# Performance work log

Measured on AMD Instinct MI355X. Metric: run time of the kernel, lower is better.

The kernel has to match this reference:

```python
import jax, jax.numpy as jnp
import numpy as np

NUM_HEADS = 16
KEY_SIZE = 64
VALUE_SIZE = 64
D_MODEL = 1024
B, S = 2, 2048

def setup_inputs() -> dict:
    key = jax.random.key(0)
    k1, k2 = jax.random.split(key)
    inputs = jax.random.normal(k1, (B, S, D_MODEL), dtype=jnp.float32)
    qkv_width = NUM_HEADS * (KEY_SIZE + KEY_SIZE + VALUE_SIZE)  # 3072
    W = jax.random.normal(k2, (D_MODEL, qkv_width), dtype=jnp.float32) / np.sqrt(D_MODEL)
    b = jnp.zeros((qkv_width,), dtype=jnp.float32)
    return {"inputs": inputs, "W": W, "b": b}

def reference(inputs, W, b):
    # Fused QKV projection: [B, S, H*(2k+v)]
    qkv = jnp.einsum("bsd,de->bse", inputs, W) + b
    Bsz, S_ = inputs.shape[0], inputs.shape[1]
    qkv = qkv.reshape(Bsz, S_, NUM_HEADS, 2 * KEY_SIZE + VALUE_SIZE)
    qkv = jnp.transpose(qkv, (0, 2, 1, 3))  # [B, H, S, 2k+v]
    q = qkv[..., :KEY_SIZE]
    k = qkv[..., KEY_SIZE:2 * KEY_SIZE]
    v = qkv[..., 2 * KEY_SIZE:]
    # NOTE: original multiplies by sqrt(key_size) (not divide) -- faithful.
    scores = jnp.einsum("bhqd,bhkd->bhqk", q, k) * jnp.sqrt(jnp.float32(KEY_SIZE))
    weights = jax.nn.softmax(scores, axis=-1)
    out = jnp.einsum("bhqk,bhkv->bhqv", weights, v)  # [B, H, S, v]
    out = jnp.transpose(out, (0, 2, 1, 3)).reshape(Bsz, S_, NUM_HEADS * VALUE_SIZE)
    return out
```

## Files before the change

kernel.cpp:

```cpp
#include <hip/hip_runtime.h>


#define S_LEN 2048
#define NH    16
#define DH    64
#define DM    1024
#define EW    3072
#define NROWS 4096
#define NT    32

#define QSCALE 11.5415603f

using f32x4 = __attribute__((ext_vector_type(4))) float;
using bf8   = __attribute__((ext_vector_type(8))) short;
using s4v   = __attribute__((ext_vector_type(4))) short;

static __device__ __forceinline__ short f2bf(float f) {
  union { float f; unsigned u; } a; a.f = f;
  unsigned r = a.u + 0x7fffu + ((a.u >> 16) & 1u);
  return (short)(r >> 16);
}
static __device__ __forceinline__ float bf2f(short h) {
  union { float f; unsigned u; } a;
  a.u = ((unsigned)(unsigned short)h) << 16;
  return a.f;
}
static __device__ __forceinline__ unsigned fbits(float f) {
  union { float f; unsigned u; } a; a.f = f; return a.u;
}
static __device__ __forceinline__ void gl16(const void* g, void* l) {
  __builtin_amdgcn_global_load_lds(
      (const __attribute__((address_space(1))) void*)g,
      (__attribute__((address_space(3))) void*)l, 16, 0, 0);
}

__global__ __launch_bounds__(256) void prep_x(const float* __restrict__ X,
                                              short* __restrict__ Xh,
                                              short* __restrict__ Xl) {
  int i = blockIdx.x * 256 + threadIdx.x;
  float4 v = ((const float4*)X)[i];
  s4v h, l;
  h.x = f2bf(v.x); l.x = f2bf(v.x - bf2f(h.x));
  h.y = f2bf(v.y); l.y = f2bf(v.y - bf2f(h.y));
  h.z = f2bf(v.z); l.z = f2bf(v.z - bf2f(h.z));
  h.w = f2bf(v.w); l.w = f2bf(v.w - bf2f(h.w));
  ((s4v*)Xh)[i] = h;
  ((s4v*)Xl)[i] = l;
}

__global__ __launch_bounds__(256) void prep_w(const float* __restrict__ W,
                                              short* __restrict__ Wth,
                                              short* __restrict__ Wtl) {
  __shared__ float t[32][33];
  int n0 = blockIdx.x * 32;
  int k0 = blockIdx.y * 32;
  int tx = threadIdx.x & 31;
  int ty = threadIdx.x >> 5;
#pragma unroll
  for (int i = 0; i < 32; i += 8)
    t[ty + i][tx] = W[(size_t)(k0 + ty + i) * EW + n0 + tx];
  __syncthreads();
#pragma unroll
  for (int i = 0; i < 32; i += 8) {
    float v = t[tx][ty + i];
    int n = n0 + ty + i;
    int h = n / 192, e = n - h * 192;
    int np = (e < 64) ? (h * 64 + e)
           : (e < 128) ? (1024 + h * 64 + (e - 64))
                       : (2048 + h * 64 + (e - 128));
    short hi = f2bf(v);
    short lo = f2bf(v - bf2f(hi));
    size_t o = (size_t)np * DM + k0 + tx;
    Wth[o] = hi; Wtl[o] = lo;
  }
}

__global__ __launch_bounds__(256, 2) void proj_qk(
    const short* __restrict__ Xh, const short* __restrict__ Xl,
    const short* __restrict__ Wth, const short* __restrict__ Wtl,
    const float* __restrict__ bias,
    short* __restrict__ Qh, short* __restrict__ Ql,
    short* __restrict__ Kh, short* __restrict__ Kl) {
  __shared__ short Ah[2][4096], Al[2][4096], Bh[2][4096], Bl[2][4096];
  const int tid = threadIdx.x;
  const int lane = tid & 63, w = tid >> 6;
  const int wr = w >> 1, wc = w & 1;
  const int c = lane & 15, g = lane >> 4;

  const int id = blockIdx.x;
  const int t = id >> 3;
  const int rowBase = (((id & 7) << 2) + (t & 3)) * 128;
  const int colBase = (t >> 2) * 128;

  f32x4 acc[4][4] = {};

  const int sr  = 32 * w + (lane >> 2);
  const int csw = ((lane & 3) ^ ((lane >> 3) & 3)) * 8;
  const int ldsw = w * 1024;
  const size_t aBase = (size_t)(rowBase + sr) * DM + csw;
  const size_t bBase = (size_t)(colBase + sr) * DM + csw;

  const int rsw = (g ^ ((c >> 1) & 3)) * 8;

#define PSTAGE(B, kt) do {                                    \
    gl16(&Xh[aBase + (kt)],            &Ah[B][ldsw]);         \
    gl16(&Xh[aBase + (kt) + 16 * DM],  &Ah[B][ldsw + 512]);   \
    gl16(&Xl[aBase + (kt)],            &Al[B][ldsw]);         \
    gl16(&Xl[aBase + (kt) + 16 * DM],  &Al[B][ldsw + 512]);   \
    gl16(&Wth[bBase + (kt)],           &Bh[B][ldsw]);         \
    gl16(&Wth[bBase + (kt) + 16 * DM], &Bh[B][ldsw + 512]);   \
    gl16(&Wtl[bBase + (kt)],           &Bl[B][ldsw]);         \
    gl16(&Wtl[bBase + (kt) + 16 * DM], &Bl[B][ldsw + 512]);   \
  } while (0)

  PSTAGE(0, 0);
  __syncthreads();

  for (int it = 0; it < 32; ++it) {
    const int cur = it & 1;

    bf8 ah[4], al4[4], bh[4], bl[4];
#pragma unroll
    for (int m = 0; m < 4; ++m) {
      int ro = (wr * 64 + m * 16 + c) * 32 + rsw;
      ah[m]  = *(const bf8*)&Ah[cur][ro];
      al4[m] = *(const bf8*)&Al[cur][ro];
    }
#pragma unroll
    for (int n = 0; n < 4; ++n) {
      int ro = (wc * 64 + n * 16 + c) * 32 + rsw;
      bh[n] = *(const bf8*)&Bh[cur][ro];
      bl[n] = *(const bf8*)&Bl[cur][ro];
    }
    if (it + 1 < 32) PSTAGE(cur ^ 1, (it + 1) * 32);

    __builtin_amdgcn_s_setprio(1);
#pragma unroll
    for (int m = 0; m < 4; ++m)
#pragma unroll
      for (int n = 0; n < 4; ++n) {
        acc[m][n] = __builtin_amdgcn_mfma_f32_16x16x32_bf16(al4[m], bh[n], acc[m][n], 0, 0, 0);
        acc[m][n] = __builtin_amdgcn_mfma_f32_16x16x32_bf16(ah[m], bl[n], acc[m][n], 0, 0, 0);
        acc[m][n] = __builtin_amdgcn_mfma_f32_16x16x32_bf16(ah[m], bh[n], acc[m][n], 0, 0, 0);
      }
    __builtin_amdgcn_s_setprio(0);
    __syncthreads();
  }
#undef PSTAGE

#pragma unroll
  for (int m = 0; m < 4; ++m)
#pragma unroll
    for (int n = 0; n < 4; ++n)
#pragma unroll
      for (int j = 0; j < 4; ++j) {
        int grow = rowBase + wr * 64 + m * 16 + g * 4 + j;
        int gcol = colBase + wc * 64 + n * 16 + c;
        int h = (gcol >> 6) & 15, e = gcol & 63;
        int bb = grow >> 11, s = grow & 2047;
        size_t hb = (size_t)(bb * NH + h);
        if (gcol < 1024) {
          float q8 = (acc[m][n][j] + bias[h * 192 + e]) * QSCALE;
          short hi = f2bf(q8);
          short lo = f2bf(q8 - bf2f(hi));
          size_t idx = (hb * S_LEN + s) * DH + e;
          Qh[idx] = hi; Ql[idx] = lo;
        } else {
          float v = acc[m][n][j] + bias[h * 192 + 64 + e];
          short hi = f2bf(v);
          short lo = f2bf(v - bf2f(hi));
          int tile = s >> 6, r = s & 63;
          size_t idx = ((hb * NT + tile) * (size_t)4096) + r * 64 +
                       ((((e >> 3) ^ (r & 7)) << 3) | (e & 7));
          Kh[idx] = hi; Kl[idx] = lo;
        }
      }
}

__global__ __launch_bounds__(256, 2) void proj_v(
    const short* __restrict__ Xh, const short* __restrict__ Wth,
    const float* __restrict__ bias, short* __restrict__ Vt) {
  __shared__ short Ah[2][4096], Bh[2][4096];
  const int tid = threadIdx.x;
  const int lane = tid & 63, w = tid >> 6;
  const int wr = w >> 1, wc = w & 1;
  const int c = lane & 15, g = lane >> 4;

  const int id = blockIdx.x;
  const int t = id >> 3;
  const int rowBase = (((id & 7) << 2) + (t & 3)) * 128;
  const int colBase = 2048 + (t >> 2) * 128;

  f32x4 acc[4][4] = {};

  const int sr  = 32 * w + (lane >> 2);
  const int csw = ((lane & 3) ^ ((lane >> 3) & 3)) * 8;
  const int ldsw = w * 1024;
  const size_t aBase = (size_t)(rowBase + sr) * DM + csw;
  const size_t bBase = (size_t)(colBase + sr) * DM + csw;
  const int rsw = (g ^ ((c >> 1) & 3)) * 8;

#define VSTAGE(B, kt) do {                                    \
    gl16(&Xh[aBase + (kt)],            &Ah[B][ldsw]);         \
    gl16(&Xh[aBase + (kt) + 16 * DM],  &Ah[B][ldsw + 512]);   \
    gl16(&Wth[bBase + (kt)],           &Bh[B][ldsw]);         \
    gl16(&Wth[bBase + (kt) + 16 * DM], &Bh[B][ldsw + 512]);   \
  } while (0)

  VSTAGE(0, 0);
  __syncthreads();

  for (int it = 0; it < 32; ++it) {
    const int cur = it & 1;
    bf8 ah[4], bh[4];
#pragma unroll
    for (int m = 0; m < 4; ++m)
      ah[m] = *(const bf8*)&Ah[cur][(wr * 64 + m * 16 + c) * 32 + rsw];
#pragma unroll
    for (int n = 0; n < 4; ++n)
      bh[n] = *(const bf8*)&Bh[cur][(wc * 64 + n * 16 + c) * 32 + rsw];
    if (it + 1 < 32) VSTAGE(cur ^ 1, (it + 1) * 32);

    __builtin_amdgcn_s_setprio(1);
#pragma unroll
    for (int m = 0; m < 4; ++m)
#pragma unroll
      for (int n = 0; n < 4; ++n)
        acc[m][n] = __builtin_amdgcn_mfma_f32_16x16x32_bf16(ah[m], bh[n], acc[m][n], 0, 0, 0);
    __builtin_amdgcn_s_setprio(0);
    __syncthreads();
  }
#undef VSTAGE

#pragma unroll
  for (int m = 0; m < 4; ++m)
#pragma unroll
    for (int n = 0; n < 4; ++n)
#pragma unroll
      for (int j = 0; j < 4; ++j) {
        int grow = rowBase + wr * 64 + m * 16 + g * 4 + j;
        int gcol = colBase + wc * 64 + n * 16 + c;
        int h = (gcol >> 6) & 15, d = gcol & 63;
        int bb = grow >> 11, s = grow & 2047;
        size_t hb = (size_t)(bb * NH + h);
        float v = acc[m][n][j] + bias[h * 192 + 128 + d];
        int tile = s >> 6, key = s & 63;
        int kc = key >> 5, g4 = (key >> 2) & 3;
        int ii = (((key >> 4) & 1) << 2) | (key & 3);
        size_t idx = ((hb * NT + tile) * (size_t)4096) + d * 64 +
                     (((((kc << 2) | g4) ^ (d & 7)) << 3) | ii);
        Vt[idx] = f2bf(v);
      }
}

__global__ __launch_bounds__(512, 4) void attn(
    const short* __restrict__ Qh, const short* __restrict__ Ql,
    const short* __restrict__ KhG, const short* __restrict__ KlG,
    const short* __restrict__ VtG, float* __restrict__ out) {
  __shared__ short KHs[2][4096];
  __shared__ short KLs[2][4096];
  __shared__ short Vs[2][4096];

  const int tid = threadIdx.x;
  const int lane = tid & 63, w = tid >> 6;
  const int c = lane & 15, g = lane >> 4;
  const int id = blockIdx.x;
  const int lid = (id & 7) * 64 + (id >> 3);
  const int bh = lid >> 4;
  const int q0 = (lid & 15) * 128 + w * 16;
  const size_t qBase  = (size_t)bh * S_LEN * DH;
  const size_t kvBase = (size_t)bh * NT * 4096;

  const int seg = tid * 8;

  bf8 qh[2], ql[2];
#pragma unroll
  for (int kc = 0; kc < 2; ++kc) {
    size_t idx = qBase + (size_t)(q0 + c) * DH + kc * 32 + g * 8;
    qh[kc] = *(const bf8*)&Qh[idx];
    ql[kc] = *(const bf8*)&Ql[idx];
  }

  int koff[2][4];
#pragma unroll
  for (int kc = 0; kc < 2; ++kc)
#pragma unroll
    for (int i = 0; i < 4; ++i)
      koff[kc][i] = (i * 16 + c) * 64 + (((kc * 4 + g) ^ (c & 7)) << 3);

  float mrun = -INFINITY, lpart = 0.f;
  f32x4 o[4] = {};

  gl16(&KhG[kvBase + seg], &KHs[0][seg]);
  gl16(&KlG[kvBase + seg], &KLs[0][seg]);
  gl16(&VtG[kvBase + seg], &Vs[0][seg]);
  __syncthreads();

  for (int t = 0; t < NT; ++t) {
    const int cur = t & 1, nxt = cur ^ 1;
    if (t + 1 < NT) {
      size_t tb = kvBase + (size_t)(t + 1) * 4096 + seg;
      gl16(&KhG[tb], &KHs[nxt][seg]);
      gl16(&KlG[tb], &KLs[nxt][seg]);
      gl16(&VtG[tb], &Vs[nxt][seg]);
    }
    const short* KH = &KHs[cur][0];
    const short* KL = &KLs[cur][0];
    const short* VV = &Vs[cur][0];

    f32x4 sc[4];
    __builtin_amdgcn_s_setprio(1);
#pragma unroll
    for (int nb = 0; nb < 4; ++nb) {
      f32x4 s = {};
#pragma unroll
      for (int kc = 0; kc < 2; ++kc) {
        bf8 kh = *(const bf8*)&KH[koff[kc][nb]];
        bf8 kl = *(const bf8*)&KL[koff[kc][nb]];
        s = __builtin_amdgcn_mfma_f32_16x16x32_bf16(kh, ql[kc], s, 0, 0, 0);
        s = __builtin_amdgcn_mfma_f32_16x16x32_bf16(kl, qh[kc], s, 0, 0, 0);
        s = __builtin_amdgcn_mfma_f32_16x16x32_bf16(kh, qh[kc], s, 0, 0, 0);
      }
      sc[nb] = s;
    }
    __builtin_amdgcn_s_setprio(0);

    float m0 = fmaxf(fmaxf(sc[0][0], sc[0][1]), fmaxf(sc[0][2], sc[0][3]));
#pragma unroll
    for (int nb = 1; nb < 4; ++nb)
      m0 = fmaxf(m0, fmaxf(fmaxf(sc[nb][0], sc[nb][1]),
                           fmaxf(sc[nb][2], sc[nb][3])));
    m0 = fmaxf(m0, __shfl_xor(m0, 16));
    m0 = fmaxf(m0, __shfl_xor(m0, 32));

    if (__any(m0 > mrun + 8.0f)) {
      float mnew = fmaxf(mrun, m0);
      float scale = exp2f(mrun - mnew);
      mrun = mnew;
      lpart *= scale;
      int sb = (g << 4) | (g << 2);
      float s0 = __shfl(scale, sb);
      float s1 = __shfl(scale, sb + 1);
      float s2 = __shfl(scale, sb + 2);
      float s3 = __shfl(scale, sb + 3);
#pragma unroll
      for (int db = 0; db < 4; ++db) {
        o[db][0] *= s0; o[db][1] *= s1; o[db][2] *= s2; o[db][3] *= s3;
      }
    }

#pragma unroll
    for (int nb = 0; nb < 4; ++nb)
#pragma unroll
      for (int j = 0; j < 4; ++j)
        sc[nb][j] = exp2f(sc[nb][j] - mrun);
#pragma unroll
    for (int nb = 0; nb < 4; ++nb)
      lpart += (sc[nb][0] + sc[nb][1]) + (sc[nb][2] + sc[nb][3]);

    union { bf8 v; unsigned u[4]; } pa[2];
#pragma unroll
    for (int kc = 0; kc < 2; ++kc) {
      pa[kc].u[0] = (fbits(sc[2*kc][0]) >> 16)   | (fbits(sc[2*kc][1])   & 0xffff0000u);
      pa[kc].u[1] = (fbits(sc[2*kc][2]) >> 16)   | (fbits(sc[2*kc][3])   & 0xffff0000u);
      pa[kc].u[2] = (fbits(sc[2*kc+1][0]) >> 16) | (fbits(sc[2*kc+1][1]) & 0xffff0000u);
      pa[kc].u[3] = (fbits(sc[2*kc+1][2]) >> 16) | (fbits(sc[2*kc+1][3]) & 0xffff0000u);
    }

    __builtin_amdgcn_s_setprio(1);
#pragma unroll
    for (int kc = 0; kc < 2; ++kc)
#pragma unroll
      for (int db = 0; db < 4; ++db) {
        bf8 vb = *(const bf8*)&VV[koff[kc][db]];
        o[db] = __builtin_amdgcn_mfma_f32_16x16x32_bf16(pa[kc].v, vb, o[db], 0, 0, 0);
      }
    __builtin_amdgcn_s_setprio(0);

    __syncthreads();
  }

  lpart += __shfl_xor(lpart, 16);
  lpart += __shfl_xor(lpart, 32);
  int sb = (g << 4) | (g << 2);
  float r0 = 1.f / __shfl(lpart, sb);
  float r1 = 1.f / __shfl(lpart, sb + 1);
  float r2 = 1.f / __shfl(lpart, sb + 2);
  float r3 = 1.f / __shfl(lpart, sb + 3);

  const int b = bh >> 4, h = bh & 15;
#pragma unroll
  for (int db = 0; db < 4; ++db) {
    int col = h * DH + db * 16 + c;
    out[((size_t)b * S_LEN + q0 + g * 4 + 0) * DM + col] = o[db][0] * r0;
    out[((size_t)b * S_LEN + q0 + g * 4 + 1) * DM + col] = o[db][1] * r1;
    out[((size_t)b * S_LEN + q0 + g * 4 + 2) * DM + col] = o[db][2] * r2;
    out[((size_t)b * S_LEN + q0 + g * 4 + 3) * DM + col] = o[db][3] * r3;
  }
}

extern "C" void kernel_launch(void* const* d_in, const int* in_sizes, int n_in,
                              void* d_out, int out_size, void* d_ws, size_t ws_size,
                              hipStream_t stream) {
  const float* X    = (const float*)d_in[0];
  const float* W    = (const float*)d_in[1];
  const float* bias = (const float*)d_in[2];
  float* out = (float*)d_out;

  char* ws = (char*)d_ws;
  size_t off = 0;
  auto take = [&](size_t bytes) {
    void* p = ws + off;
    off += (bytes + 255) & ~(size_t)255;
    return p;
  };
  short* Xh  = (short*)take((size_t)NROWS * DM * 2);
  short* Xl  = (short*)take((size_t)NROWS * DM * 2);
  short* Wth = (short*)take((size_t)EW * DM * 2);
  short* Wtl = (short*)take((size_t)EW * DM * 2);
  short* Qh  = (short*)take((size_t)2 * NH * S_LEN * DH * 2);
  short* Ql  = (short*)take((size_t)2 * NH * S_LEN * DH * 2);
  short* Kh  = (short*)take((size_t)2 * NH * NT * 4096 * 2);
  short* Kl  = (short*)take((size_t)2 * NH * NT * 4096 * 2);
  short* Vt  = (short*)take((size_t)2 * NH * NT * 4096 * 2);

  prep_x<<<dim3(4096), dim3(256), 0, stream>>>(X, Xh, Xl);
  prep_w<<<dim3(EW / 32, DM / 32), dim3(256), 0, stream>>>(W, Wth, Wtl);
  proj_qk<<<dim3(512), dim3(256), 0, stream>>>(
      Xh, Xl, Wth, Wtl, bias, Qh, Ql, Kh, Kl);
  proj_v<<<dim3(256), dim3(256), 0, stream>>>(Xh, Wth, bias, Vt);
  attn<<<dim3(512), dim3(512), 0, stream>>>(
      Qh, Ql, Kh, Kl, Vt, out);
}
```

Before: 174.5 us.

## Pre-swizzle W into MFMA fragment layout and load B operands directly to registers

prep_w now writes the bf16 weight halves in a fragment-major layout matching the MFMA B operand. The projection kernels read B straight from global memory into registers, one k-step ahead, instead of staging it through LDS, which halves LDS traffic and footprint. The low half of W is no longer written for V columns, and the main loop is unrolled by two. Separately, the attention P-matrix packing switches from truncating bit masks to the v_cvt_pk_bf16_f32 instruction, which rounds to nearest, slightly changing numerics. Each lane's 16-byte global loads are contiguous in the new layout, but register pressure rises from holding two sets of B fragments.

After: 174.6 us. About the same (+0.0%).

```diff
diff --git a/kernel.cpp b/kernel.cpp
--- a/kernel.cpp
+++ b/kernel.cpp
@@ -24,9 +24,6 @@
   union { float f; unsigned u; } a;
   a.u = ((unsigned)(unsigned short)h) << 16;
   return a.f;
-}
-static __device__ __forceinline__ unsigned fbits(float f) {
-  union { float f; unsigned u; } a; a.f = f; return a.u;
 }
 static __device__ __forceinline__ void gl16(const void* g, void* l) {
   __builtin_amdgcn_global_load_lds(
@@ -49,8 +46,8 @@
 }
 
 __global__ __launch_bounds__(256) void prep_w(const float* __restrict__ W,
-                                              short* __restrict__ Wth,
-                                              short* __restrict__ Wtl) {
+                                              short* __restrict__ Wfh,
+                                              short* __restrict__ Wfl) {
   __shared__ float t[32][33];
   int n0 = blockIdx.x * 32;
   int k0 = blockIdx.y * 32;
@@ -60,6 +57,7 @@
   for (int i = 0; i < 32; i += 8)
     t[ty + i][tx] = W[(size_t)(k0 + ty + i) * EW + n0 + tx];
   __syncthreads();
+  const int kt = k0 >> 5;
 #pragma unroll
   for (int i = 0; i < 32; i += 8) {
     float v = t[tx][ty + i];
@@ -68,20 +66,22 @@
     int np = (e < 64) ? (h * 64 + e)
            : (e < 128) ? (1024 + h * 64 + (e - 64))
                        : (2048 + h * 64 + (e - 128));
+    int n16 = np >> 4, c = np & 15;
+    int gg = (tx >> 3) & 3, ee = tx & 7;
+    size_t o = ((size_t)(n16 * 32 + kt)) * 512 + (gg * 16 + c) * 8 + ee;
     short hi = f2bf(v);
-    short lo = f2bf(v - bf2f(hi));
-    size_t o = (size_t)np * DM + k0 + tx;
-    Wth[o] = hi; Wtl[o] = lo;
+    Wfh[o] = hi;
+    if (np < 2048) Wfl[o] = f2bf(v - bf2f(hi));
   }
 }
 
 __global__ __launch_bounds__(256, 2) void proj_qk(
     const short* __restrict__ Xh, const short* __restrict__ Xl,
-    const short* __restrict__ Wth, const short* __restrict__ Wtl,
+    const short* __restrict__ Wfh, const short* __restrict__ Wfl,
     const float* __restrict__ bias,
     short* __restrict__ Qh, short* __restrict__ Ql,
     short* __restrict__ Kh, short* __restrict__ Kl) {
-  __shared__ short Ah[2][4096], Al[2][4096], Bh[2][4096], Bl[2][4096];
+  __shared__ short Ah[2][4096], Al[2][4096];
   const int tid = threadIdx.x;
   const int lane = tid & 63, w = tid >> 6;
   const int wr = w >> 1, wc = w & 1;
@@ -98,55 +98,74 @@
   const int csw = ((lane & 3) ^ ((lane >> 3) & 3)) * 8;
   const int ldsw = w * 1024;
   const size_t aBase = (size_t)(rowBase + sr) * DM + csw;
-  const size_t bBase = (size_t)(colBase + sr) * DM + csw;
-
   const int rsw = (g ^ ((c >> 1) & 3)) * 8;
 
-#define PSTAGE(B, kt) do {                                    \
+  size_t bB[4];
+#pragma unroll
+  for (int n = 0; n < 4; ++n)
+    bB[n] = ((size_t)((colBase >> 4) + wc * 4 + n) * 32) * 512 + lane * 8;
+
+#define ASTAGE(B, kt) do {                                    \
     gl16(&Xh[aBase + (kt)],            &Ah[B][ldsw]);         \
     gl16(&Xh[aBase + (kt) + 16 * DM],  &Ah[B][ldsw + 512]);   \
     gl16(&Xl[aBase + (kt)],            &Al[B][ldsw]);         \
     gl16(&Xl[aBase + (kt) + 16 * DM],  &Al[B][ldsw + 512]);   \
-    gl16(&Wth[bBase + (kt)],           &Bh[B][ldsw]);         \
-    gl16(&Wth[bBase + (kt) + 16 * DM], &Bh[B][ldsw + 512]);   \
-    gl16(&Wtl[bBase + (kt)],           &Bl[B][ldsw]);         \
-    gl16(&Wtl[bBase + (kt) + 16 * DM], &Bl[B][ldsw + 512]);   \
   } while (0)
-
-  PSTAGE(0, 0);
+#define LOADB(dh, dl, kt) do {                                \
+    _Pragma("unroll")                                         \
+    for (int n = 0; n < 4; ++n) {                             \
+      dh[n] = *(const bf8*)&Wfh[bB[n] + (size_t)(kt) * 512];  \
+      dl[n] = *(const bf8*)&Wfl[bB[n] + (size_t)(kt) * 512];  \
+    }                                                         \
+  } while (0)
+#define QKMFMA(bh, bl) do {                                   \
+    _Pragma("unroll")                                         \
+    for (int m = 0; m < 4; ++m) {                             \
+      _Pragma("unroll")                                       \
+      for (int n = 0; n < 4; ++n) {                           \
+        acc[m][n] = __builtin_amdgcn_mfma_f32_16x16x32_bf16(al4[m], bh[n], acc[m][n], 0, 0, 0); \
+        acc[m][n] = __builtin_amdgcn_mfma_f32_16x16x32_bf16(ah[m], bl[n], acc[m][n], 0, 0, 0);  \
+        acc[m][n] = __builtin_amdgcn_mfma_f32_16x16x32_bf16(ah[m], bh[n], acc[m][n], 0, 0, 0);  \
+      }                                                       \
+    }                                                         \
+  } while (0)
+
+  bf8 b0h[4], b0l[4], b1h[4], b1l[4];
+  LOADB(b0h, b0l, 0);
+  ASTAGE(0, 0);
   __syncthreads();
 
-  for (int it = 0; it < 32; ++it) {
-    const int cur = it & 1;
-
-    bf8 ah[4], al4[4], bh[4], bl[4];
+  for (int it = 0; it < 32; it += 2) {
+    LOADB(b1h, b1l, it + 1);
+    bf8 ah[4], al4[4];
 #pragma unroll
     for (int m = 0; m < 4; ++m) {
       int ro = (wr * 64 + m * 16 + c) * 32 + rsw;
-      ah[m]  = *(const bf8*)&Ah[cur][ro];
-      al4[m] = *(const bf8*)&Al[cur][ro];
-    }
-#pragma unroll
-    for (int n = 0; n < 4; ++n) {
-      int ro = (wc * 64 + n * 16 + c) * 32 + rsw;
-      bh[n] = *(const bf8*)&Bh[cur][ro];
-      bl[n] = *(const bf8*)&Bl[cur][ro];
-    }
-    if (it + 1 < 32) PSTAGE(cur ^ 1, (it + 1) * 32);
-
-    __builtin_amdgcn_s_setprio(1);
-#pragma unroll
-    for (int m = 0; m < 4; ++m)
-#pragma unroll
-      for (int n = 0; n < 4; ++n) {
-        acc[m][n] = __builtin_amdgcn_mfma_f32_16x16x32_bf16(al4[m], bh[n], acc[m][n], 0, 0, 0);
-        acc[m][n] = __builtin_amdgcn_mfma_f32_16x16x32_bf16(ah[m], bl[n], acc[m][n], 0, 0, 0);
-        acc[m][n] = __builtin_amdgcn_mfma_f32_16x16x32_bf16(ah[m], bh[n], acc[m][n], 0, 0, 0);
-      }
+      ah[m]  = *(const bf8*)&Ah[0][ro];
+      al4[m] = *(const bf8*)&Al[0][ro];
+    }
+    ASTAGE(1, (it + 1) * 32);
+    __builtin_amdgcn_s_setprio(1);
+    QKMFMA(b0h, b0l);
     __builtin_amdgcn_s_setprio(0);
     __syncthreads();
-  }
-#undef PSTAGE
+
+    if (it + 2 < 32) LOADB(b0h, b0l, it + 2);
+#pragma unroll
+    for (int m = 0; m < 4; ++m) {
+      int ro = (wr * 64 + m * 16 + c) * 32 + rsw;
+      ah[m]  = *(const bf8*)&Ah[1][ro];
+      al4[m] = *(const bf8*)&Al[1][ro];
+    }
+    if (it + 2 < 32) ASTAGE(0, (it + 2) * 32);
+    __builtin_amdgcn_s_setprio(1);
+    QKMFMA(b1h, b1l);
+    __builtin_amdgcn_s_setprio(0);
+    __syncthreads();
+  }
+#undef ASTAGE
+#undef LOADB
+#undef QKMFMA
 
 #pragma unroll
   for (int m = 0; m < 4; ++m)
@@ -178,9 +197,9 @@
 }
 
 __global__ __launch_bounds__(256, 2) void proj_v(
-    const short* __restrict__ Xh, const short* __restrict__ Wth,
+    const short* __restrict__ Xh, const short* __restrict__ Wfh,
     const float* __restrict__ bias, short* __restrict__ Vt) {
-  __shared__ short Ah[2][4096], Bh[2][4096];
+  __shared__ short Ah[2][4096];
   const int tid = threadIdx.x;
   const int lane = tid & 63, w = tid >> 6;
   const int wr = w >> 1, wc = w & 1;
@@ -197,40 +216,60 @@
   const int csw = ((lane & 3) ^ ((lane >> 3) & 3)) * 8;
   const int ldsw = w * 1024;
   const size_t aBase = (size_t)(rowBase + sr) * DM + csw;
-  const size_t bBase = (size_t)(colBase + sr) * DM + csw;
   const int rsw = (g ^ ((c >> 1) & 3)) * 8;
 
-#define VSTAGE(B, kt) do {                                    \
+  size_t bB[4];
+#pragma unroll
+  for (int n = 0; n < 4; ++n)
+    bB[n] = ((size_t)((colBase >> 4) + wc * 4 + n) * 32) * 512 + lane * 8;
+
+#define VASTAGE(B, kt) do {                                   \
     gl16(&Xh[aBase + (kt)],            &Ah[B][ldsw]);         \
     gl16(&Xh[aBase + (kt) + 16 * DM],  &Ah[B][ldsw + 512]);   \
-    gl16(&Wth[bBase + (kt)],           &Bh[B][ldsw]);         \
-    gl16(&Wth[bBase + (kt) + 16 * DM], &Bh[B][ldsw + 512]);   \
   } while (0)
-
-  VSTAGE(0, 0);
+#define VLOADB(dh, kt) do {                                   \
+    _Pragma("unroll")                                         \
+    for (int n = 0; n < 4; ++n)                               \
+      dh[n] = *(const bf8*)&Wfh[bB[n] + (size_t)(kt) * 512];  \
+  } while (0)
+
+  bf8 b0h[4], b1h[4];
+  VLOADB(b0h, 0);
+  VASTAGE(0, 0);
   __syncthreads();
 
-  for (int it = 0; it < 32; ++it) {
-    const int cur = it & 1;
-    bf8 ah[4], bh[4];
+  for (int it = 0; it < 32; it += 2) {
+    VLOADB(b1h, it + 1);
+    bf8 ah[4];
 #pragma unroll
     for (int m = 0; m < 4; ++m)
-      ah[m] = *(const bf8*)&Ah[cur][(wr * 64 + m * 16 + c) * 32 + rsw];
-#pragma unroll
-    for (int n = 0; n < 4; ++n)
-      bh[n] = *(const bf8*)&Bh[cur][(wc * 64 + n * 16 + c) * 32 + rsw];
-    if (it + 1 < 32) VSTAGE(cur ^ 1, (it + 1) * 32);
-
+      ah[m] = *(const bf8*)&Ah[0][(wr * 64 + m * 16 + c) * 32 + rsw];
+    VASTAGE(1, (it + 1) * 32);
     __builtin_amdgcn_s_setprio(1);
 #pragma unroll
     for (int m = 0; m < 4; ++m)
 #pragma unroll
       for (int n = 0; n < 4; ++n)
-        acc[m][n] = __builtin_amdgcn_mfma_f32_16x16x32_bf16(ah[m], bh[n], acc[m][n], 0, 0, 0);
+        acc[m][n] = __builtin_amdgcn_mfma_f32_16x16x32_bf16(ah[m], b0h[n], acc[m][n], 0, 0, 0);
     __builtin_amdgcn_s_setprio(0);
     __syncthreads();
-  }
-#undef VSTAGE
+
+    if (it + 2 < 32) VLOADB(b0h, it + 2);
+#pragma unroll
+    for (int m = 0; m < 4; ++m)
+      ah[m] = *(const bf8*)&Ah[1][(wr * 64 + m * 16 + c) * 32 + rsw];
+    if (it + 2 < 32) VASTAGE(0, (it + 2) * 32);
+    __builtin_amdgcn_s_setprio(1);
+#pragma unroll
+    for (int m = 0; m < 4; ++m)
+#pragma unroll
+      for (int n = 0; n < 4; ++n)
+        acc[m][n] = __builtin_amdgcn_mfma_f32_16x16x32_bf16(ah[m], b1h[n], acc[m][n], 0, 0, 0);
+    __builtin_amdgcn_s_setprio(0);
+    __syncthreads();
+  }
+#undef VASTAGE
+#undef VLOADB
 
 #pragma unroll
   for (int m = 0; m < 4; ++m)
@@ -361,10 +400,14 @@
     union { bf8 v; unsigned u[4]; } pa[2];
 #pragma unroll
     for (int kc = 0; kc < 2; ++kc) {
-      pa[kc].u[0] = (fbits(sc[2*kc][0]) >> 16)   | (fbits(sc[2*kc][1])   & 0xffff0000u);
-      pa[kc].u[1] = (fbits(sc[2*kc][2]) >> 16)   | (fbits(sc[2*kc][3])   & 0xffff0000u);
-      pa[kc].u[2] = (fbits(sc[2*kc+1][0]) >> 16) | (fbits(sc[2*kc+1][1]) & 0xffff0000u);
-      pa[kc].u[3] = (fbits(sc[2*kc+1][2]) >> 16) | (fbits(sc[2*kc+1][3]) & 0xffff0000u);
+      asm("v_cvt_pk_bf16_f32 %0, %1, %2"
+          : "=v"(pa[kc].u[0]) : "v"(sc[2 * kc][0]), "v"(sc[2 * kc][1]));
+      asm("v_cvt_pk_bf16_f32 %0, %1, %2"
+          : "=v"(pa[kc].u[1]) : "v"(sc[2 * kc][2]), "v"(sc[2 * kc][3]));
+      asm("v_cvt_pk_bf16_f32 %0, %1, %2"
+          : "=v"(pa[kc].u[2]) : "v"(sc[2 * kc + 1][0]), "v"(sc[2 * kc + 1][1]));
+      asm("v_cvt_pk_bf16_f32 %0, %1, %2"
+          : "=v"(pa[kc].u[3]) : "v"(sc[2 * kc + 1][2]), "v"(sc[2 * kc + 1][3]));
     }
 
     __builtin_amdgcn_s_setprio(1);
@@ -416,8 +459,8 @@
   };
   short* Xh  = (short*)take((size_t)NROWS * DM * 2);
   short* Xl  = (short*)take((size_t)NROWS * DM * 2);
-  short* Wth = (short*)take((size_t)EW * DM * 2);
-  short* Wtl = (short*)take((size_t)EW * DM * 2);
+  short* Wfh = (short*)take((size_t)EW * DM * 2);
+  short* Wfl = (short*)take((size_t)EW * DM * 2);
   short* Qh  = (short*)take((size_t)2 * NH * S_LEN * DH * 2);
   short* Ql  = (short*)take((size_t)2 * NH * S_LEN * DH * 2);
   short* Kh  = (short*)take((size_t)2 * NH * NT * 4096 * 2);
@@ -425,10 +468,10 @@
   short* Vt  = (short*)take((size_t)2 * NH * NT * 4096 * 2);
 
   prep_x<<<dim3(4096), dim3(256), 0, stream>>>(X, Xh, Xl);
-  prep_w<<<dim3(EW / 32, DM / 32), dim3(256), 0, stream>>>(W, Wth, Wtl);
+  prep_w<<<dim3(EW / 32, DM / 32), dim3(256), 0, stream>>>(W, Wfh, Wfl);
   proj_qk<<<dim3(512), dim3(256), 0, stream>>>(
-      Xh, Xl, Wth, Wtl, bias, Qh, Ql, Kh, Kl);
-  proj_v<<<dim3(256), dim3(256), 0, stream>>>(Xh, Wth, bias, Vt);
+      Xh, Xl, Wfh, Wfl, bias, Qh, Ql, Kh, Kl);
+  proj_v<<<dim3(256), dim3(256), 0, stream>>>(Xh, Wfh, bias, Vt);
   attn<<<dim3(512), dim3(512), 0, stream>>>(
       Qh, Ql, Kh, Kl, Vt, out);
 }
```
